# Optimization experiments

Measured on AMD Instinct MI355X. Metric: run time of the kernel, lower is better.

The kernel has to match this reference:

```python
import jax, jax.numpy as jnp
import numpy as np

B, T, C_EMB, C_HEAD = 4, 4096, 1024, 64

def setup_inputs() -> dict:
    key = jax.random.key(0)
    kx, kk, kq, kv = jax.random.split(key, 4)
    x = jax.random.normal(kx, (B, T, C_EMB), dtype=jnp.float32)
    # nn.Linear(C_EMB, C_HEAD, bias=False); store as (in, out) so projection is x @ W
    Wk = jax.random.normal(kk, (C_EMB, C_HEAD), dtype=jnp.float32) * 0.02
    Wq = jax.random.normal(kq, (C_EMB, C_HEAD), dtype=jnp.float32) * 0.02
    Wv = jax.random.normal(kv, (C_EMB, C_HEAD), dtype=jnp.float32) * 0.02
    return {"x": x, "Wk": Wk, "Wq": Wq, "Wv": Wv}

def reference(x, Wk, Wq, Wv):
    k = x @ Wk  # [B,T,Ch]
    q = x @ Wq
    v = x @ Wv
    scale = C_HEAD ** -0.5
    weights = jnp.einsum('bqc,bkc->bqk', q, k) * scale  # [B,T,T]
    causal = jnp.tril(jnp.ones((T, T), dtype=bool))
    weights = jnp.where(causal, weights, -jnp.inf)
    # NOTE: original uses F.softmax(dim=1), i.e. over the QUERY (row) axis -> axis=-2
    weights = jax.nn.softmax(weights, axis=-2)
    # dropout_rate=0.0 (eval) -> identity
    return jnp.einsum('bqk,bkc->bqc', weights, v)
```

## Files before the change

kernel.cpp:

```cpp
#include <hip/hip_runtime.h>
#include <math.h>

#define BB 4
#define TT 4096
#define CE 1024
#define CH 64
#define SCALE2 0.18033688011112042f
#define NQT 64
#define NZ 4

typedef unsigned short ushort_t;
typedef __attribute__((ext_vector_type(8))) short bf16x8;
typedef __attribute__((ext_vector_type(8))) unsigned short u16x8;
typedef __attribute__((ext_vector_type(4))) float f32x4;

__device__ __forceinline__ unsigned short f2bf(float f) {
    unsigned int x = __builtin_bit_cast(unsigned int, f);
    unsigned int r = x + 0x7fffu + ((x >> 16) & 1u);
    return (unsigned short)(r >> 16);
}
__device__ __forceinline__ float bf2f(unsigned short u) {
    unsigned int x = ((unsigned int)u) << 16;
    return __builtin_bit_cast(float, x);
}

__device__ __forceinline__ void stage_tile(const ushort_t* __restrict__ src,
                                           ushort_t (*dst)[68], int tid)
{
#pragma unroll
    for (int i = 0; i < 2; ++i) {
        const int idx = i * 256 + tid;
        const int row = idx >> 3, c0 = (idx & 7) * 8;
        u16x8 v = *(const u16x8*)(src + (long)idx * 8);
        union { u16x8 v; uint2 q[2]; } uu; uu.v = v;
        *(uint2*)&dst[row][c0]     = uu.q[0];
        *(uint2*)&dst[row][c0 + 4] = uu.q[1];
    }
}

__device__ __forceinline__ bf16x8 frag68(const ushort_t* p) {
    union { bf16x8 v; uint2 q[2]; } uu;
    uu.q[0] = *(const uint2*)p;
    uu.q[1] = *(const uint2*)(p + 4);
    return uu.v;
}

__global__ __launch_bounds__(256)
void wt_build(const float* __restrict__ Wk, const float* __restrict__ Wq,
              const float* __restrict__ Wv, ushort_t* __restrict__ wt2)
{
    const int m = blockIdx.x, kt = blockIdx.y;
    const float* __restrict__ W = (m == 0) ? Wk : (m == 1 ? Wq : Wv);
    const int k0 = kt * 64;
    __shared__ float lds[64][65];
    const int cc = threadIdx.x & 63, g = threadIdx.x >> 6;
#pragma unroll
    for (int i = 0; i < 16; ++i) {
        const int r = g * 16 + i;
        lds[r][cc] = W[(k0 + r) * CH + cc];
    }
    __syncthreads();
    const int k = k0 + cc;
#pragma unroll
    for (int i = 0; i < 16; ++i) {
        const int c = g * 16 + i;
        wt2[((long)(k >> 5) * 192 + (m * 64 + c)) * 32 + (k & 31)] = f2bf(lds[cc][c]);
    }
}

__global__ __launch_bounds__(512)
void proj_mfma(const float* __restrict__ x, const ushort_t* __restrict__ wt2,
               ushort_t* __restrict__ qb, ushort_t* __restrict__ kb, ushort_t* __restrict__ vb)
{
    const int tid = threadIdx.x;
    const int w = tid >> 6, l = tid & 63, lg = l >> 4, lr = l & 15;
    const int wr = w >> 2, wc = w & 3;
    const long t0 = (long)blockIdx.x * 32;

    __shared__ ushort_t As[32][68];
    __shared__ ushort_t Bs[192][68];

    f32x4 acc[3];
#pragma unroll
    for (int nf = 0; nf < 3; ++nf) acc[nf] = (f32x4){0.f, 0.f, 0.f, 0.f};

    const int arow = tid >> 4, acol = (tid & 15) * 4;
    const float* __restrict__ xsrc = x + (t0 + arow) * CE + acol;

    int bc[3], bh[3], bk[3];
#pragma unroll
    for (int i = 0; i < 3; ++i) {
        const int idx = i * 512 + tid;
        const int h = idx >= 768;
        const int j = idx - h * 768;
        bc[i] = j >> 2; bh[i] = h; bk[i] = (j & 3) * 8;
    }

    float4 a4 = *(const float4*)(xsrc);
    u16x8 bv[3];
#pragma unroll
    for (int i = 0; i < 3; ++i)
        bv[i] = *(const u16x8*)(wt2 + ((long)(bh[i]) * 192 + bc[i]) * 32 + bk[i]);

    for (int step = 0; step < 16; ++step) {
        {
            uint2 pk;
            pk.x = (unsigned)f2bf(a4.x) | ((unsigned)f2bf(a4.y) << 16);
            pk.y = (unsigned)f2bf(a4.z) | ((unsigned)f2bf(a4.w) << 16);
            *(uint2*)&As[arow][acol] = pk;
#pragma unroll
            for (int i = 0; i < 3; ++i) {
                union { u16x8 v; uint2 q[2]; } uu; uu.v = bv[i];
                ushort_t* d = &Bs[bc[i]][bh[i] * 32 + bk[i]];
                *(uint2*)d = uu.q[0];
                *(uint2*)(d + 4) = uu.q[1];
            }
        }
        __syncthreads();
        if (step < 15) {
            const int k0n = (step + 1) * 64;
            a4 = *(const float4*)(xsrc + k0n);
            const int ktn = k0n >> 5;
#pragma unroll
            for (int i = 0; i < 3; ++i)
                bv[i] = *(const u16x8*)(wt2 + ((long)(ktn + bh[i]) * 192 + bc[i]) * 32 + bk[i]);
        }
#pragma unroll
        for (int h = 0; h < 2; ++h) {
            bf16x8 af = frag68(&As[wr * 16 + lr][h * 32 + lg * 8]);
#pragma unroll
            for (int nf = 0; nf < 3; ++nf) {
                bf16x8 bf = frag68(&Bs[wc * 48 + nf * 16 + lr][h * 32 + lg * 8]);
                acc[nf] = __builtin_amdgcn_mfma_f32_16x16x32_bf16(af, bf, acc[nf], 0, 0, 0);
            }
        }
        __syncthreads();
    }

    ushort_t* Os = &Bs[0][0];
#pragma unroll
    for (int nf = 0; nf < 3; ++nf)
#pragma unroll
        for (int r = 0; r < 4; ++r)
            Os[(wr * 16 + lg * 4 + r) * 200 + wc * 48 + nf * 16 + lr] = f2bf(acc[nf][r]);
    __syncthreads();
    if (tid < 256) {
        const int row = tid >> 3, c0 = (tid & 7) * 8;
#pragma unroll
        for (int m = 0; m < 3; ++m) {
            u16x8 ov = *(const u16x8*)&Os[row * 200 + m * 64 + c0];
            ushort_t* __restrict__ outp = (m == 0) ? kb : (m == 1 ? qb : vb);
            *(u16x8*)(outp + (t0 + row) * CH + c0) = ov;
        }
    }
}

__global__ __launch_bounds__(256)
void colstats_mfma(const ushort_t* __restrict__ qb, const ushort_t* __restrict__ kb,
                   float* __restrict__ pl)
{
    const int b = blockIdx.x, p = blockIdx.y, z = blockIdx.z;
    const int tid = threadIdx.x;
    const int w = tid >> 6, l = tid & 63, lg = l >> 4, lr = l & 15;
    const long baseT = (long)b * TT;
    const long NTT = (long)BB * TT;

    __shared__ ushort_t Ks[64][68], Qs[64][68];

    for (int pass = 0; pass < 2; ++pass) {
        const int kt = pass ? (63 - p) : p;
        stage_tile(kb + (baseT + (long)kt * 64) * CH, Ks, tid);
        __syncthreads();
        bf16x8 ka0 = frag68(&Ks[w * 16 + lr][lg * 8]);
        bf16x8 ka1 = frag68(&Ks[w * 16 + lr][32 + lg * 8]);

        float l_r[4] = {0.f, 0.f, 0.f, 0.f};

        const int j0 = kt + ((z - kt) & (NZ - 1));
        for (int j = j0; j < NQT; j += NZ) {
            stage_tile(qb + (baseT + (long)j * 64) * CH, Qs, tid);
            __syncthreads();
            const bool diag = (j == kt);
#pragma unroll
            for (int qf = 0; qf < 4; ++qf) {
                bf16x8 b0 = frag68(&Qs[qf * 16 + lr][lg * 8]);
                bf16x8 b1 = frag68(&Qs[qf * 16 + lr][32 + lg * 8]);
                f32x4 s = {0.f, 0.f, 0.f, 0.f};
                s = __builtin_amdgcn_mfma_f32_16x16x32_bf16(ka0, b0, s, 0, 0, 0);
                s = __builtin_amdgcn_mfma_f32_16x16x32_bf16(ka1, b1, s, 0, 0, 0);
#pragma unroll
                for (int r = 0; r < 4; ++r) {
                    float ev = exp2f(s[r] * SCALE2);
                    if (diag && (qf * 16 + lr) < (w * 16 + lg * 4 + r)) ev = 0.f;
                    l_r[r] += ev;
                }
            }
            __syncthreads();
        }
#pragma unroll
        for (int r = 0; r < 4; ++r) {
            float lv = l_r[r];
            for (int d = 1; d < 16; d <<= 1) lv += __shfl_xor(lv, d);
            if (lr == 0) {
                const long k = (long)kt * 64 + w * 16 + lg * 4 + r;
                pl[(long)z * NTT + baseT + k] = lv;
            }
        }
    }
}

__global__ __launch_bounds__(256)
void vt_scale(const ushort_t* __restrict__ vb, const float* __restrict__ pl,
              ushort_t* __restrict__ vtb2)
{
    const int b = blockIdx.x;
    const int jt = blockIdx.y;
    const long t0 = (long)jt * 64;
    const int tid = threadIdx.x;
    __shared__ ushort_t lds[64][72];
    const long baseT = (long)b * TT;
    const long NTT = (long)BB * TT;
#pragma unroll
    for (int i = 0; i < 2; ++i) {
        const int t = i * 32 + (tid >> 3);
        const int c0 = (tid & 7) * 8;
        u16x8 v = *(const u16x8*)(vb + (baseT + t0 + t) * CH + c0);
        const long idx = baseT + t0 + t;
        float ls = pl[idx];
#pragma unroll
        for (int zz = 1; zz < NZ; ++zz) ls += pl[zz * NTT + idx];
        const float sc = 1.f / ls;
#pragma unroll
        for (int j = 0; j < 8; ++j) lds[c0 + j][t] = f2bf(bf2f(v[j]) * sc);
    }
    __syncthreads();
    ushort_t* __restrict__ dst = vtb2 + ((long)(b * 64 + jt)) * (64 * 64);
#pragma unroll
    for (int i = 0; i < 2; ++i) {
        const int c = i * 32 + (tid >> 3);
        const int tt0 = (tid & 7) * 8;
        u16x8 ov = *(const u16x8*)&lds[c][tt0];
        *(u16x8*)(dst + (long)c * 64 + tt0) = ov;
    }
}

__global__ __launch_bounds__(256)
void pv_mfma(const ushort_t* __restrict__ qb, const ushort_t* __restrict__ kb,
             const ushort_t* __restrict__ vtb2, float* __restrict__ pout)
{
    const int b = blockIdx.x, p = blockIdx.y, z = blockIdx.z;
    const int tid = threadIdx.x;
    const int w = tid >> 6, l = tid & 63, lg = l >> 4, lr = l & 15;
    const long baseT = (long)b * TT;
    const long NTT = (long)BB * TT;

    __shared__ ushort_t Qs[64][68], Ks[64][68], Vs[64][68], Ps[64][68];

    for (int pass = 0; pass < 2; ++pass) {
        const int qt = pass ? (63 - p) : p;
        stage_tile(qb + (baseT + (long)qt * 64) * CH, Qs, tid);
        __syncthreads();
        bf16x8 qf_[4][2];
#pragma unroll
        for (int qf = 0; qf < 4; ++qf) {
            qf_[qf][0] = frag68(&Qs[qf * 16 + lr][lg * 8]);
            qf_[qf][1] = frag68(&Qs[qf * 16 + lr][32 + lg * 8]);
        }
        f32x4 o[4];
#pragma unroll
        for (int qf = 0; qf < 4; ++qf) o[qf] = (f32x4){0.f, 0.f, 0.f, 0.f};

        for (int j = z; j <= qt; j += NZ) {
            stage_tile(kb + (baseT + (long)j * 64) * CH, Ks, tid);
            stage_tile(vtb2 + ((long)(b * 64 + j)) * (64 * 64), Vs, tid);
            __syncthreads();
            bf16x8 ka0 = frag68(&Ks[w * 16 + lr][lg * 8]);
            bf16x8 ka1 = frag68(&Ks[w * 16 + lr][32 + lg * 8]);
            bf16x8 va0 = frag68(&Vs[w * 16 + lr][lg * 8]);
            bf16x8 va1 = frag68(&Vs[w * 16 + lr][32 + lg * 8]);
            const bool diag = (j == qt);
#pragma unroll
            for (int qf = 0; qf < 4; ++qf) {
                f32x4 s = {0.f, 0.f, 0.f, 0.f};
                s = __builtin_amdgcn_mfma_f32_16x16x32_bf16(ka0, qf_[qf][0], s, 0, 0, 0);
                s = __builtin_amdgcn_mfma_f32_16x16x32_bf16(ka1, qf_[qf][1], s, 0, 0, 0);
                unsigned short e[4];
#pragma unroll
                for (int r = 0; r < 4; ++r) {
                    float ev = exp2f(s[r] * SCALE2);
                    if (diag && (qf * 16 + lr) < (w * 16 + lg * 4 + r)) ev = 0.f;
                    e[r] = f2bf(ev);
                }
                uint2 pk;
                pk.x = (unsigned)e[0] | ((unsigned)e[1] << 16);
                pk.y = (unsigned)e[2] | ((unsigned)e[3] << 16);
                *(uint2*)&Ps[qf * 16 + lr][w * 16 + lg * 4] = pk;
            }
            __syncthreads();
#pragma unroll
            for (int qf = 0; qf < 4; ++qf) {
                bf16x8 p0 = frag68(&Ps[qf * 16 + lr][lg * 8]);
                bf16x8 p1 = frag68(&Ps[qf * 16 + lr][32 + lg * 8]);
                o[qf] = __builtin_amdgcn_mfma_f32_16x16x32_bf16(va0, p0, o[qf], 0, 0, 0);
                o[qf] = __builtin_amdgcn_mfma_f32_16x16x32_bf16(va1, p1, o[qf], 0, 0, 0);
            }
        }
        float* pz = pout + ((long)z * NTT + baseT + (long)qt * 64) * CH;
#pragma unroll
        for (int qf = 0; qf < 4; ++qf)
            *(f32x4*)(pz + (long)(qf * 16 + lr) * CH + w * 16 + lg * 4) = o[qf];
    }
}

__global__ __launch_bounds__(256)
void finalize_out(const float* __restrict__ pout, float* __restrict__ out)
{
    const long i = (long)blockIdx.x * 256 + threadIdx.x;
    const long n4 = (long)BB * TT * CH / 4;
    float4 r = reinterpret_cast<const float4*>(pout)[i];
#pragma unroll
    for (int zz = 1; zz < NZ; ++zz) {
        float4 a = reinterpret_cast<const float4*>(pout)[zz * n4 + i];
        r.x += a.x; r.y += a.y; r.z += a.z; r.w += a.w;
    }
    reinterpret_cast<float4*>(out)[i] = r;
}

extern "C" void kernel_launch(void* const* d_in, const int* in_sizes, int n_in,
                              void* d_out, int out_size, void* d_ws, size_t ws_size,
                              hipStream_t stream)
{
    const float* x  = (const float*)d_in[0];
    const float* Wk = (const float*)d_in[1];
    const float* Wq = (const float*)d_in[2];
    const float* Wv = (const float*)d_in[3];
    float* out = (float*)d_out;

    const size_t NT = (size_t)BB * TT;
    ushort_t* qb   = (ushort_t*)d_ws;
    ushort_t* kb   = qb + NT * CH;
    ushort_t* vb   = kb + NT * CH;
    ushort_t* vtb2 = vb + NT * CH;
    ushort_t* wt2  = vtb2 + NT * CH;
    float* pl   = (float*)(wt2 + 192 * CE);
    float* pout = pl + NZ * NT;

    hipLaunchKernelGGL(wt_build, dim3(3, 16), dim3(256), 0, stream,
                       Wk, Wq, Wv, wt2);
    hipLaunchKernelGGL(proj_mfma, dim3(NT / 32), dim3(512), 0, stream,
                       x, wt2, qb, kb, vb);
    hipLaunchKernelGGL(colstats_mfma, dim3(BB, NQT / 2, NZ), dim3(256), 0, stream,
                       qb, kb, pl);
    hipLaunchKernelGGL(vt_scale, dim3(BB, TT / 64), dim3(256), 0, stream,
                       vb, pl, vtb2);
    hipLaunchKernelGGL(pv_mfma, dim3(BB, NQT / 2, NZ), dim3(256), 0, stream,
                       qb, kb, vtb2, pout);
    hipLaunchKernelGGL(finalize_out, dim3(NT * CH / 4 / 256), dim3(256), 0, stream,
                       pout, out);
}
```

Measured before the change: 89.35 us.

## Split key/query tile loops across two wave groups in colstats and pv kernels

Both the column-statistics and PV kernels now launch 512 threads per block. Two groups of four waves each process alternating j tiles in separate shared-memory buffers. At the end, the partial row sums and output accumulators are reduced through shared memory. This roughly halves the serial loop length per block and doubles the waves in flight. The cost is more LDS per block, extra barriers with idle waves on odd iteration counts, and a final cross-group reduction.

```diff
diff --git a/kernel.cpp b/kernel.cpp
--- a/kernel.cpp
+++ b/kernel.cpp
@@ -25,17 +25,27 @@
 }
 
 __device__ __forceinline__ void stage_tile(const ushort_t* __restrict__ src,
-                                           ushort_t (*dst)[68], int tid)
+                                           ushort_t (*dst)[68], int tg)
 {
 #pragma unroll
     for (int i = 0; i < 2; ++i) {
-        const int idx = i * 256 + tid;
+        const int idx = i * 256 + tg;
         const int row = idx >> 3, c0 = (idx & 7) * 8;
         u16x8 v = *(const u16x8*)(src + (long)idx * 8);
         union { u16x8 v; uint2 q[2]; } uu; uu.v = v;
         *(uint2*)&dst[row][c0]     = uu.q[0];
         *(uint2*)&dst[row][c0 + 4] = uu.q[1];
     }
+}
+
+__device__ __forceinline__ void stage_tile512(const ushort_t* __restrict__ src,
+                                              ushort_t (*dst)[68], int tid)
+{
+    const int row = tid >> 3, c0 = (tid & 7) * 8;
+    u16x8 v = *(const u16x8*)(src + (long)tid * 8);
+    union { u16x8 v; uint2 q[2]; } uu; uu.v = v;
+    *(uint2*)&dst[row][c0]     = uu.q[0];
+    *(uint2*)&dst[row][c0 + 4] = uu.q[1];
 }
 
 __device__ __forceinline__ bf16x8 frag68(const ushort_t* p) {
@@ -155,57 +165,72 @@
     }
 }
 
-__global__ __launch_bounds__(256)
+__global__ __launch_bounds__(512)
 void colstats_mfma(const ushort_t* __restrict__ qb, const ushort_t* __restrict__ kb,
                    float* __restrict__ pl)
 {
     const int b = blockIdx.x, p = blockIdx.y, z = blockIdx.z;
     const int tid = threadIdx.x;
     const int w = tid >> 6, l = tid & 63, lg = l >> 4, lr = l & 15;
+    const int wg = w >> 2, wc = w & 3, tg = tid & 255;
     const long baseT = (long)b * TT;
     const long NTT = (long)BB * TT;
 
-    __shared__ ushort_t Ks[64][68], Qs[64][68];
+    __shared__ ushort_t Ks[64][68], Qs[2][64][68];
+    __shared__ float redc[4][64][5];
 
     for (int pass = 0; pass < 2; ++pass) {
         const int kt = pass ? (63 - p) : p;
-        stage_tile(kb + (baseT + (long)kt * 64) * CH, Ks, tid);
-        __syncthreads();
-        bf16x8 ka0 = frag68(&Ks[w * 16 + lr][lg * 8]);
-        bf16x8 ka1 = frag68(&Ks[w * 16 + lr][32 + lg * 8]);
+        stage_tile512(kb + (baseT + (long)kt * 64) * CH, Ks, tid);
+        __syncthreads();
+        bf16x8 ka0 = frag68(&Ks[wc * 16 + lr][lg * 8]);
+        bf16x8 ka1 = frag68(&Ks[wc * 16 + lr][32 + lg * 8]);
 
         float l_r[4] = {0.f, 0.f, 0.f, 0.f};
 
         const int j0 = kt + ((z - kt) & (NZ - 1));
-        for (int j = j0; j < NQT; j += NZ) {
-            stage_tile(qb + (baseT + (long)j * 64) * CH, Qs, tid);
+        const int n0 = (j0 < NQT) ? ((NQT - 1 - j0) >> 3) + 1 : 0;
+        for (int i = 0; i < n0; ++i) {
+            const int j = j0 + 4 * wg + 8 * i;
+            const bool act = (j < NQT);
+            if (act) stage_tile(qb + (baseT + (long)j * 64) * CH, Qs[wg], tg);
             __syncthreads();
-            const bool diag = (j == kt);
-#pragma unroll
-            for (int qf = 0; qf < 4; ++qf) {
-                bf16x8 b0 = frag68(&Qs[qf * 16 + lr][lg * 8]);
-                bf16x8 b1 = frag68(&Qs[qf * 16 + lr][32 + lg * 8]);
-                f32x4 s = {0.f, 0.f, 0.f, 0.f};
-                s = __builtin_amdgcn_mfma_f32_16x16x32_bf16(ka0, b0, s, 0, 0, 0);
-                s = __builtin_amdgcn_mfma_f32_16x16x32_bf16(ka1, b1, s, 0, 0, 0);
-#pragma unroll
-                for (int r = 0; r < 4; ++r) {
-                    float ev = exp2f(s[r] * SCALE2);
-                    if (diag && (qf * 16 + lr) < (w * 16 + lg * 4 + r)) ev = 0.f;
-                    l_r[r] += ev;
+            if (act) {
+                const bool diag = (j == kt);
+#pragma unroll
+                for (int qf = 0; qf < 4; ++qf) {
+                    bf16x8 b0 = frag68(&Qs[wg][qf * 16 + lr][lg * 8]);
+                    bf16x8 b1 = frag68(&Qs[wg][qf * 16 + lr][32 + lg * 8]);
+                    f32x4 s = {0.f, 0.f, 0.f, 0.f};
+                    s = __builtin_amdgcn_mfma_f32_16x16x32_bf16(ka0, b0, s, 0, 0, 0);
+                    s = __builtin_amdgcn_mfma_f32_16x16x32_bf16(ka1, b1, s, 0, 0, 0);
+#pragma unroll
+                    for (int r = 0; r < 4; ++r) {
+                        float ev = exp2f(s[r] * SCALE2);
+                        if (diag && (qf * 16 + lr) < (wc * 16 + lg * 4 + r)) ev = 0.f;
+                        l_r[r] += ev;
+                    }
                 }
             }
             __syncthreads();
         }
-#pragma unroll
-        for (int r = 0; r < 4; ++r) {
-            float lv = l_r[r];
-            for (int d = 1; d < 16; d <<= 1) lv += __shfl_xor(lv, d);
-            if (lr == 0) {
-                const long k = (long)kt * 64 + w * 16 + lg * 4 + r;
-                pl[(long)z * NTT + baseT + k] = lv;
-            }
-        }
+        if (wg == 1) {
+#pragma unroll
+            for (int r = 0; r < 4; ++r) redc[wc][l][r] = l_r[r];
+        }
+        __syncthreads();
+        if (wg == 0) {
+#pragma unroll
+            for (int r = 0; r < 4; ++r) {
+                float lv = l_r[r] + redc[wc][l][r];
+                for (int d = 1; d < 16; d <<= 1) lv += __shfl_xor(lv, d);
+                if (lr == 0) {
+                    const long k = (long)kt * 64 + wc * 16 + lg * 4 + r;
+                    pl[(long)z * NTT + baseT + k] = lv;
+                }
+            }
+        }
+        __syncthreads();
     }
 }
 
@@ -244,21 +269,23 @@
     }
 }
 
-__global__ __launch_bounds__(256)
+__global__ __launch_bounds__(512)
 void pv_mfma(const ushort_t* __restrict__ qb, const ushort_t* __restrict__ kb,
              const ushort_t* __restrict__ vtb2, float* __restrict__ pout)
 {
     const int b = blockIdx.x, p = blockIdx.y, z = blockIdx.z;
     const int tid = threadIdx.x;
     const int w = tid >> 6, l = tid & 63, lg = l >> 4, lr = l & 15;
+    const int wg = w >> 2, wc = w & 3, tg = tid & 255;
     const long baseT = (long)b * TT;
     const long NTT = (long)BB * TT;
 
-    __shared__ ushort_t Qs[64][68], Ks[64][68], Vs[64][68], Ps[64][68];
+    __shared__ ushort_t Qs[64][68], Ks[2][64][68], Vs[2][64][68], Ps[2][64][68];
+    __shared__ float redp[4][64][17];
 
     for (int pass = 0; pass < 2; ++pass) {
         const int qt = pass ? (63 - p) : p;
-        stage_tile(qb + (baseT + (long)qt * 64) * CH, Qs, tid);
+        stage_tile512(qb + (baseT + (long)qt * 64) * CH, Qs, tid);
         __syncthreads();
         bf16x8 qf_[4][2];
 #pragma unroll
@@ -270,45 +297,69 @@
 #pragma unroll
         for (int qf = 0; qf < 4; ++qf) o[qf] = (f32x4){0.f, 0.f, 0.f, 0.f};
 
-        for (int j = z; j <= qt; j += NZ) {
-            stage_tile(kb + (baseT + (long)j * 64) * CH, Ks, tid);
-            stage_tile(vtb2 + ((long)(b * 64 + j)) * (64 * 64), Vs, tid);
+        const int n0 = (qt >= z) ? ((qt - z) >> 3) + 1 : 0;
+        for (int i = 0; i < n0; ++i) {
+            const int j = z + 4 * wg + 8 * i;
+            const bool act = (j <= qt);
+            if (act) {
+                stage_tile(kb + (baseT + (long)j * 64) * CH, Ks[wg], tg);
+                stage_tile(vtb2 + ((long)(b * 64 + j)) * (64 * 64), Vs[wg], tg);
+            }
             __syncthreads();
-            bf16x8 ka0 = frag68(&Ks[w * 16 + lr][lg * 8]);
-            bf16x8 ka1 = frag68(&Ks[w * 16 + lr][32 + lg * 8]);
-            bf16x8 va0 = frag68(&Vs[w * 16 + lr][lg * 8]);
-            bf16x8 va1 = frag68(&Vs[w * 16 + lr][32 + lg * 8]);
-            const bool diag = (j == qt);
+            bf16x8 va0, va1;
+            if (act) {
+                bf16x8 ka0 = frag68(&Ks[wg][wc * 16 + lr][lg * 8]);
+                bf16x8 ka1 = frag68(&Ks[wg][wc * 16 + lr][32 + lg * 8]);
+                va0 = frag68(&Vs[wg][wc * 16 + lr][lg * 8]);
+                va1 = frag68(&Vs[wg][wc * 16 + lr][32 + lg * 8]);
+                const bool diag = (j == qt);
+#pragma unroll
+                for (int qf = 0; qf < 4; ++qf) {
+                    f32x4 s = {0.f, 0.f, 0.f, 0.f};
+                    s = __builtin_amdgcn_mfma_f32_16x16x32_bf16(ka0, qf_[qf][0], s, 0, 0, 0);
+                    s = __builtin_amdgcn_mfma_f32_16x16x32_bf16(ka1, qf_[qf][1], s, 0, 0, 0);
+                    unsigned short e[4];
+#pragma unroll
+                    for (int r = 0; r < 4; ++r) {
+                        float ev = exp2f(s[r] * SCALE2);
+                        if (diag && (qf * 16 + lr) < (wc * 16 + lg * 4 + r)) ev = 0.f;
+                        e[r] = f2bf(ev);
+                    }
+                    uint2 pk;
+                    pk.x = (unsigned)e[0] | ((unsigned)e[1] << 16);
+                    pk.y = (unsigned)e[2] | ((unsigned)e[3] << 16);
+                    *(uint2*)&Ps[wg][qf * 16 + lr][wc * 16 + lg * 4] = pk;
+                }
+            }
+            __syncthreads();
+            if (act) {
+#pragma unroll
+                for (int qf = 0; qf < 4; ++qf) {
+                    bf16x8 p0 = frag68(&Ps[wg][qf * 16 + lr][lg * 8]);
+                    bf16x8 p1 = frag68(&Ps[wg][qf * 16 + lr][32 + lg * 8]);
+                    o[qf] = __builtin_amdgcn_mfma_f32_16x16x32_bf16(va0, p0, o[qf], 0, 0, 0);
+                    o[qf] = __builtin_amdgcn_mfma_f32_16x16x32_bf16(va1, p1, o[qf], 0, 0, 0);
+                }
+            }
+        }
+        if (wg == 1) {
+#pragma unroll
+            for (int qf = 0; qf < 4; ++qf)
+#pragma unroll
+                for (int r = 0; r < 4; ++r) redp[wc][l][qf * 4 + r] = o[qf][r];
+        }
+        __syncthreads();
+        if (wg == 0) {
+            float* pz = pout + ((long)z * NTT + baseT + (long)qt * 64) * CH;
 #pragma unroll
             for (int qf = 0; qf < 4; ++qf) {
-                f32x4 s = {0.f, 0.f, 0.f, 0.f};
-                s = __builtin_amdgcn_mfma_f32_16x16x32_bf16(ka0, qf_[qf][0], s, 0, 0, 0);
-                s = __builtin_amdgcn_mfma_f32_16x16x32_bf16(ka1, qf_[qf][1], s, 0, 0, 0);
-                unsigned short e[4];
-#pragma unroll
-                for (int r = 0; r < 4; ++r) {
-                    float ev = exp2f(s[r] * SCALE2);
-                    if (diag && (qf * 16 + lr) < (w * 16 + lg * 4 + r)) ev = 0.f;
-                    e[r] = f2bf(ev);
-                }
-                uint2 pk;
-                pk.x = (unsigned)e[0] | ((unsigned)e[1] << 16);
-                pk.y = (unsigned)e[2] | ((unsigned)e[3] << 16);
-                *(uint2*)&Ps[qf * 16 + lr][w * 16 + lg * 4] = pk;
-            }
-            __syncthreads();
-#pragma unroll
-            for (int qf = 0; qf < 4; ++qf) {
-                bf16x8 p0 = frag68(&Ps[qf * 16 + lr][lg * 8]);
-                bf16x8 p1 = frag68(&Ps[qf * 16 + lr][32 + lg * 8]);
-                o[qf] = __builtin_amdgcn_mfma_f32_16x16x32_bf16(va0, p0, o[qf], 0, 0, 0);
-                o[qf] = __builtin_amdgcn_mfma_f32_16x16x32_bf16(va1, p1, o[qf], 0, 0, 0);
-            }
-        }
-        float* pz = pout + ((long)z * NTT + baseT + (long)qt * 64) * CH;
-#pragma unroll
-        for (int qf = 0; qf < 4; ++qf)
-            *(f32x4*)(pz + (long)(qf * 16 + lr) * CH + w * 16 + lg * 4) = o[qf];
+                f32x4 ov = o[qf];
+#pragma unroll
+                for (int r = 0; r < 4; ++r) ov[r] += redp[wc][l][qf * 4 + r];
+                *(f32x4*)(pz + (long)(qf * 16 + lr) * CH + wc * 16 + lg * 4) = ov;
+            }
+        }
+        __syncthreads();
     }
 }
 
@@ -349,11 +400,11 @@
                        Wk, Wq, Wv, wt2);
     hipLaunchKernelGGL(proj_mfma, dim3(NT / 32), dim3(512), 0, stream,
                        x, wt2, qb, kb, vb);
-    hipLaunchKernelGGL(colstats_mfma, dim3(BB, NQT / 2, NZ), dim3(256), 0, stream,
+    hipLaunchKernelGGL(colstats_mfma, dim3(BB, NQT / 2, NZ), dim3(512), 0, stream,
                        qb, kb, pl);
     hipLaunchKernelGGL(vt_scale, dim3(BB, TT / 64), dim3(256), 0, stream,
                        vb, pl, vtb2);
-    hipLaunchKernelGGL(pv_mfma, dim3(BB, NQT / 2, NZ), dim3(256), 0, stream,
+    hipLaunchKernelGGL(pv_mfma, dim3(BB, NQT / 2, NZ), dim3(512), 0, stream,
                        qb, kb, vtb2, pout);
     hipLaunchKernelGGL(finalize_out, dim3(NT * CH / 4 / 256), dim3(256), 0, stream,
                        pout, out);
```

After: 75.89 us. 15.1% less time.

## Replace paired-tile blocks with one tile per block and widen colstats split

Applied to the files above, without the earlier changes.

Both attention kernels drop the two-pass pairing where each block handled tile p and tile 63-p. They now launch one block per tile. colstats also splits the query range 8 ways instead of 4, and pv_mfma orders blocks heaviest-first by mapping qt = 63 - blockIdx.y. The aim is more blocks in flight on the many-CU GPU and less per-block serial work, with hardware scheduling evening out the load. The cost is more launched blocks with uneven work, extra partial-sum traffic for the column sums, and more K tile restaging.

```diff
diff --git a/kernel.cpp b/kernel.cpp
--- a/kernel.cpp
+++ b/kernel.cpp
@@ -7,7 +7,8 @@
 #define CH 64
 #define SCALE2 0.18033688011112042f
 #define NQT 64
-#define NZ 4
+#define NZC 8
+#define NZP 4
 
 typedef unsigned short ushort_t;
 typedef __attribute__((ext_vector_type(8))) short bf16x8;
@@ -159,7 +160,7 @@
 void colstats_mfma(const ushort_t* __restrict__ qb, const ushort_t* __restrict__ kb,
                    float* __restrict__ pl)
 {
-    const int b = blockIdx.x, p = blockIdx.y, z = blockIdx.z;
+    const int b = blockIdx.x, kt = blockIdx.y, z = blockIdx.z;
     const int tid = threadIdx.x;
     const int w = tid >> 6, l = tid & 63, lg = l >> 4, lr = l & 15;
     const long baseT = (long)b * TT;
@@ -167,44 +168,41 @@
 
     __shared__ ushort_t Ks[64][68], Qs[64][68];
 
-    for (int pass = 0; pass < 2; ++pass) {
-        const int kt = pass ? (63 - p) : p;
-        stage_tile(kb + (baseT + (long)kt * 64) * CH, Ks, tid);
-        __syncthreads();
-        bf16x8 ka0 = frag68(&Ks[w * 16 + lr][lg * 8]);
-        bf16x8 ka1 = frag68(&Ks[w * 16 + lr][32 + lg * 8]);
-
-        float l_r[4] = {0.f, 0.f, 0.f, 0.f};
-
-        const int j0 = kt + ((z - kt) & (NZ - 1));
-        for (int j = j0; j < NQT; j += NZ) {
-            stage_tile(qb + (baseT + (long)j * 64) * CH, Qs, tid);
-            __syncthreads();
-            const bool diag = (j == kt);
-#pragma unroll
-            for (int qf = 0; qf < 4; ++qf) {
-                bf16x8 b0 = frag68(&Qs[qf * 16 + lr][lg * 8]);
-                bf16x8 b1 = frag68(&Qs[qf * 16 + lr][32 + lg * 8]);
-                f32x4 s = {0.f, 0.f, 0.f, 0.f};
-                s = __builtin_amdgcn_mfma_f32_16x16x32_bf16(ka0, b0, s, 0, 0, 0);
-                s = __builtin_amdgcn_mfma_f32_16x16x32_bf16(ka1, b1, s, 0, 0, 0);
-#pragma unroll
-                for (int r = 0; r < 4; ++r) {
-                    float ev = exp2f(s[r] * SCALE2);
-                    if (diag && (qf * 16 + lr) < (w * 16 + lg * 4 + r)) ev = 0.f;
-                    l_r[r] += ev;
-                }
+    stage_tile(kb + (baseT + (long)kt * 64) * CH, Ks, tid);
+    __syncthreads();
+    bf16x8 ka0 = frag68(&Ks[w * 16 + lr][lg * 8]);
+    bf16x8 ka1 = frag68(&Ks[w * 16 + lr][32 + lg * 8]);
+
+    float l_r[4] = {0.f, 0.f, 0.f, 0.f};
+
+    const int j0 = kt + ((z - kt) & (NZC - 1));
+    for (int j = j0; j < NQT; j += NZC) {
+        stage_tile(qb + (baseT + (long)j * 64) * CH, Qs, tid);
+        __syncthreads();
+        const bool diag = (j == kt);
+#pragma unroll
+        for (int qf = 0; qf < 4; ++qf) {
+            bf16x8 b0 = frag68(&Qs[qf * 16 + lr][lg * 8]);
+            bf16x8 b1 = frag68(&Qs[qf * 16 + lr][32 + lg * 8]);
+            f32x4 s = {0.f, 0.f, 0.f, 0.f};
+            s = __builtin_amdgcn_mfma_f32_16x16x32_bf16(ka0, b0, s, 0, 0, 0);
+            s = __builtin_amdgcn_mfma_f32_16x16x32_bf16(ka1, b1, s, 0, 0, 0);
+#pragma unroll
+            for (int r = 0; r < 4; ++r) {
+                float ev = exp2f(s[r] * SCALE2);
+                if (diag && (qf * 16 + lr) < (w * 16 + lg * 4 + r)) ev = 0.f;
+                l_r[r] += ev;
             }
-            __syncthreads();
-        }
-#pragma unroll
-        for (int r = 0; r < 4; ++r) {
-            float lv = l_r[r];
-            for (int d = 1; d < 16; d <<= 1) lv += __shfl_xor(lv, d);
-            if (lr == 0) {
-                const long k = (long)kt * 64 + w * 16 + lg * 4 + r;
-                pl[(long)z * NTT + baseT + k] = lv;
-            }
+        }
+        __syncthreads();
+    }
+#pragma unroll
+    for (int r = 0; r < 4; ++r) {
+        float lv = l_r[r];
+        for (int d = 1; d < 16; d <<= 1) lv += __shfl_xor(lv, d);
+        if (lr == 0) {
+            const long k = (long)kt * 64 + w * 16 + lg * 4 + r;
+            pl[(long)z * NTT + baseT + k] = lv;
         }
     }
 }
@@ -228,7 +226,7 @@
         const long idx = baseT + t0 + t;
         float ls = pl[idx];
 #pragma unroll
-        for (int zz = 1; zz < NZ; ++zz) ls += pl[zz * NTT + idx];
+        for (int zz = 1; zz < NZC; ++zz) ls += pl[zz * NTT + idx];
         const float sc = 1.f / ls;
 #pragma unroll
         for (int j = 0; j < 8; ++j) lds[c0 + j][t] = f2bf(bf2f(v[j]) * sc);
@@ -248,7 +246,8 @@
 void pv_mfma(const ushort_t* __restrict__ qb, const ushort_t* __restrict__ kb,
              const ushort_t* __restrict__ vtb2, float* __restrict__ pout)
 {
-    const int b = blockIdx.x, p = blockIdx.y, z = blockIdx.z;
+    const int b = blockIdx.x, z = blockIdx.z;
+    const int qt = 63 - blockIdx.y;
     const int tid = threadIdx.x;
     const int w = tid >> 6, l = tid & 63, lg = l >> 4, lr = l & 15;
     const long baseT = (long)b * TT;
@@ -256,60 +255,57 @@
 
     __shared__ ushort_t Qs[64][68], Ks[64][68], Vs[64][68], Ps[64][68];
 
-    for (int pass = 0; pass < 2; ++pass) {
-        const int qt = pass ? (63 - p) : p;
-        stage_tile(qb + (baseT + (long)qt * 64) * CH, Qs, tid);
-        __syncthreads();
-        bf16x8 qf_[4][2];
+    stage_tile(qb + (baseT + (long)qt * 64) * CH, Qs, tid);
+    __syncthreads();
+    bf16x8 qf_[4][2];
+#pragma unroll
+    for (int qf = 0; qf < 4; ++qf) {
+        qf_[qf][0] = frag68(&Qs[qf * 16 + lr][lg * 8]);
+        qf_[qf][1] = frag68(&Qs[qf * 16 + lr][32 + lg * 8]);
+    }
+    f32x4 o[4];
+#pragma unroll
+    for (int qf = 0; qf < 4; ++qf) o[qf] = (f32x4){0.f, 0.f, 0.f, 0.f};
+
+    for (int j = z; j <= qt; j += NZP) {
+        stage_tile(kb + (baseT + (long)j * 64) * CH, Ks, tid);
+        stage_tile(vtb2 + ((long)(b * 64 + j)) * (64 * 64), Vs, tid);
+        __syncthreads();
+        bf16x8 ka0 = frag68(&Ks[w * 16 + lr][lg * 8]);
+        bf16x8 ka1 = frag68(&Ks[w * 16 + lr][32 + lg * 8]);
+        bf16x8 va0 = frag68(&Vs[w * 16 + lr][lg * 8]);
+        bf16x8 va1 = frag68(&Vs[w * 16 + lr][32 + lg * 8]);
+        const bool diag = (j == qt);
 #pragma unroll
         for (int qf = 0; qf < 4; ++qf) {
-            qf_[qf][0] = frag68(&Qs[qf * 16 + lr][lg * 8]);
-            qf_[qf][1] = frag68(&Qs[qf * 16 + lr][32 + lg * 8]);
-        }
-        f32x4 o[4];
-#pragma unroll
-        for (int qf = 0; qf < 4; ++qf) o[qf] = (f32x4){0.f, 0.f, 0.f, 0.f};
-
-        for (int j = z; j <= qt; j += NZ) {
-            stage_tile(kb + (baseT + (long)j * 64) * CH, Ks, tid);
-            stage_tile(vtb2 + ((long)(b * 64 + j)) * (64 * 64), Vs, tid);
-            __syncthreads();
-            bf16x8 ka0 = frag68(&Ks[w * 16 + lr][lg * 8]);
-            bf16x8 ka1 = frag68(&Ks[w * 16 + lr][32 + lg * 8]);
-            bf16x8 va0 = frag68(&Vs[w * 16 + lr][lg * 8]);
-            bf16x8 va1 = frag68(&Vs[w * 16 + lr][32 + lg * 8]);
-            const bool diag = (j == qt);
-#pragma unroll
-            for (int qf = 0; qf < 4; ++qf) {
-                f32x4 s = {0.f, 0.f, 0.f, 0.f};
-                s = __builtin_amdgcn_mfma_f32_16x16x32_bf16(ka0, qf_[qf][0], s, 0, 0, 0);
-                s = __builtin_amdgcn_mfma_f32_16x16x32_bf16(ka1, qf_[qf][1], s, 0, 0, 0);
-                unsigned short e[4];
-#pragma unroll
-                for (int r = 0; r < 4; ++r) {
-                    float ev = exp2f(s[r] * SCALE2);
-                    if (diag && (qf * 16 + lr) < (w * 16 + lg * 4 + r)) ev = 0.f;
-                    e[r] = f2bf(ev);
-                }
-                uint2 pk;
-                pk.x = (unsigned)e[0] | ((unsigned)e[1] << 16);
-                pk.y = (unsigned)e[2] | ((unsigned)e[3] << 16);
-                *(uint2*)&Ps[qf * 16 + lr][w * 16 + lg * 4] = pk;
+            f32x4 s = {0.f, 0.f, 0.f, 0.f};
+            s = __builtin_amdgcn_mfma_f32_16x16x32_bf16(ka0, qf_[qf][0], s, 0, 0, 0);
+            s = __builtin_amdgcn_mfma_f32_16x16x32_bf16(ka1, qf_[qf][1], s, 0, 0, 0);
+            unsigned short e[4];
+#pragma unroll
+            for (int r = 0; r < 4; ++r) {
+                float ev = exp2f(s[r] * SCALE2);
+                if (diag && (qf * 16 + lr) < (w * 16 + lg * 4 + r)) ev = 0.f;
+                e[r] = f2bf(ev);
             }
-            __syncthreads();
-#pragma unroll
-            for (int qf = 0; qf < 4; ++qf) {
-                bf16x8 p0 = frag68(&Ps[qf * 16 + lr][lg * 8]);
-                bf16x8 p1 = frag68(&Ps[qf * 16 + lr][32 + lg * 8]);
-                o[qf] = __builtin_amdgcn_mfma_f32_16x16x32_bf16(va0, p0, o[qf], 0, 0, 0);
-                o[qf] = __builtin_amdgcn_mfma_f32_16x16x32_bf16(va1, p1, o[qf], 0, 0, 0);
-            }
-        }
-        float* pz = pout + ((long)z * NTT + baseT + (long)qt * 64) * CH;
-#pragma unroll
-        for (int qf = 0; qf < 4; ++qf)
-            *(f32x4*)(pz + (long)(qf * 16 + lr) * CH + w * 16 + lg * 4) = o[qf];
-    }
+            uint2 pk;
+            pk.x = (unsigned)e[0] | ((unsigned)e[1] << 16);
+            pk.y = (unsigned)e[2] | ((unsigned)e[3] << 16);
+            *(uint2*)&Ps[qf * 16 + lr][w * 16 + lg * 4] = pk;
+        }
+        __syncthreads();
+#pragma unroll
+        for (int qf = 0; qf < 4; ++qf) {
+            bf16x8 p0 = frag68(&Ps[qf * 16 + lr][lg * 8]);
+            bf16x8 p1 = frag68(&Ps[qf * 16 + lr][32 + lg * 8]);
+            o[qf] = __builtin_amdgcn_mfma_f32_16x16x32_bf16(va0, p0, o[qf], 0, 0, 0);
+            o[qf] = __builtin_amdgcn_mfma_f32_16x16x32_bf16(va1, p1, o[qf], 0, 0, 0);
+        }
+    }
+    float* pz = pout + ((long)z * NTT + baseT + (long)qt * 64) * CH;
+#pragma unroll
+    for (int qf = 0; qf < 4; ++qf)
+        *(f32x4*)(pz + (long)(qf * 16 + lr) * CH + w * 16 + lg * 4) = o[qf];
 }
 
 __global__ __launch_bounds__(256)
@@ -319,7 +315,7 @@
     const long n4 = (long)BB * TT * CH / 4;
     float4 r = reinterpret_cast<const float4*>(pout)[i];
 #pragma unroll
-    for (int zz = 1; zz < NZ; ++zz) {
+    for (int zz = 1; zz < NZP; ++zz) {
         float4 a = reinterpret_cast<const float4*>(pout)[zz * n4 + i];
         r.x += a.x; r.y += a.y; r.z += a.z; r.w += a.w;
     }
@@ -343,17 +339,17 @@
     ushort_t* vtb2 = vb + NT * CH;
     ushort_t* wt2  = vtb2 + NT * CH;
     float* pl   = (float*)(wt2 + 192 * CE);
-    float* pout = pl + NZ * NT;
+    float* pout = pl + NZC * NT;
 
     hipLaunchKernelGGL(wt_build, dim3(3, 16), dim3(256), 0, stream,
                        Wk, Wq, Wv, wt2);
     hipLaunchKernelGGL(proj_mfma, dim3(NT / 32), dim3(512), 0, stream,
                        x, wt2, qb, kb, vb);
-    hipLaunchKernelGGL(colstats_mfma, dim3(BB, NQT / 2, NZ), dim3(256), 0, stream,
+    hipLaunchKernelGGL(colstats_mfma, dim3(BB, NQT, NZC), dim3(256), 0, stream,
                        qb, kb, pl);
     hipLaunchKernelGGL(vt_scale, dim3(BB, TT / 64), dim3(256), 0, stream,
                        vb, pl, vtb2);
-    hipLaunchKernelGGL(pv_mfma, dim3(BB, NQT / 2, NZ), dim3(256), 0, stream,
+    hipLaunchKernelGGL(pv_mfma, dim3(BB, NQT, NZP), dim3(256), 0, stream,
                        qb, kb, vtb2, pout);
     hipLaunchKernelGGL(finalize_out, dim3(NT * CH / 4 / 256), dim3(256), 0, stream,
                        pout, out);
```

Result: slower. 93.48 us (+4.6%).
